# Performance work log

Measured on AMD Instinct MI355X. Metric: run time of the kernel, lower is better.

Reference implementation:

```python
import jax, jax.numpy as jnp
import numpy as np

E = 1024      # embed_dim
H = 16        # num heads
D = E // H    # head_dim = 64
B, T = 4, 2048


def setup_inputs() -> dict:
    key = jax.random.key(0)
    ks = jax.random.split(key, 7)
    hidden_states = jax.random.normal(ks[0], (B, T, E), dtype=jnp.float32)
    # torch Linear weight layout: [out_features, in_features]
    Wqkv = jax.random.normal(ks[1], (3 * E, E), dtype=jnp.float32) * (1.0 / np.sqrt(E))
    bqkv = jax.random.normal(ks[2], (3 * E,), dtype=jnp.float32) * 0.02
    Wproj = jax.random.normal(ks[3], (E, E), dtype=jnp.float32) * (1.0 / np.sqrt(E))
    bproj = jax.random.normal(ks[4], (E,), dtype=jnp.float32) * 0.02
    splat_scale = jax.random.normal(ks[5], (H,), dtype=jnp.float32) * 0.5
    splat_bias = jax.random.normal(ks[6], (H, 1, 1), dtype=jnp.float32) * 0.5
    return {
        'hidden_states': hidden_states,
        'Wqkv': Wqkv, 'bqkv': bqkv,
        'Wproj': Wproj, 'bproj': bproj,
        'splat_scale': splat_scale, 'splat_bias': splat_bias,
    }


def reference(hidden_states, Wqkv, bqkv, Wproj, bproj, splat_scale, splat_bias):
    b, t, _ = hidden_states.shape
    scale_factor = 1.0 / np.sqrt(D)

    qkv = hidden_states @ Wqkv.T + bqkv                    # [B,T,3E]
    q, k, v = jnp.split(qkv, 3, axis=-1)
    # [B,H,T,D]
    q = q.reshape(b, t, H, D).transpose(0, 2, 1, 3)
    k = k.reshape(b, t, H, D).transpose(0, 2, 1, 3)
    v = v.reshape(b, t, H, D).transpose(0, 2, 1, 3)

    scores = jnp.einsum('bhqd,bhkd->bhqk', q * scale_factor, k)  # [B,H,T,T]

    s = (1.0 + 0.01 * jnp.tanh(splat_scale)).reshape(1, H, 1, 1)
    bsp = (0.001 * jnp.tanh(splat_bias)).reshape(1, H, 1, 1)
    scores = s * scores + bsp

    causal = jnp.tril(jnp.ones((t, t), dtype=bool))
    scores = jnp.where(causal, scores, jnp.float32(-1e9))

    attn = jax.nn.softmax(scores, axis=-1)                 # dropout = identity (eval)
    out = jnp.einsum('bhqk,bhkd->bhqd', attn, v)
    out = out.transpose(0, 2, 1, 3).reshape(b, t, E)
    out = out @ Wproj.T + bproj
    return out
```

## Files before the change

kernel.cpp:

```cpp
#include <hip/hip_runtime.h>
#include <stdint.h>

#define BB 4
#define TT 2048
#define EE 1024
#define HH 16
#define DD 64
#define MM (BB*TT)
#define NQKV (3*EE)

typedef __bf16 bf16_t;
typedef bf16_t bf16x8 __attribute__((ext_vector_type(8)));
typedef short  s16x4  __attribute__((ext_vector_type(4)));
typedef float  floatx4 __attribute__((ext_vector_type(4)));

__device__ __forceinline__ unsigned short f2bf(float f) {
    unsigned int u = __float_as_uint(f);
    u = (u + 0x7FFFu + ((u >> 16) & 1u)) >> 16;
    return (unsigned short)u;
}

__device__ __forceinline__ void load_lds16(const void* g, void* l) {
    __builtin_amdgcn_global_load_lds(
        (const __attribute__((address_space(1))) unsigned int*)g,
        (__attribute__((address_space(3))) unsigned int*)l, 16, 0, 0);
}

__global__ void cvt_f32_bf16(const float* __restrict__ in,
                             unsigned short* __restrict__ out, int n) {
    int i = (blockIdx.x * 256 + threadIdx.x) * 4;
    if (i + 3 < n) {
        float4 v = *reinterpret_cast<const float4*>(in + i);
        ushort4 o;
        o.x = f2bf(v.x); o.y = f2bf(v.y); o.z = f2bf(v.z); o.w = f2bf(v.w);
        *reinterpret_cast<ushort4*>(out + i) = o;
    }
}

#define VW(N) asm volatile("s_waitcnt vmcnt(" #N ")" ::: "memory")
#define BARX() do { __builtin_amdgcn_s_barrier(); asm volatile("" ::: "memory"); } while (0)
#define FR(p, t) (*reinterpret_cast<const bf16x8*>((p) + (t) * 512))
#define MFMA1(mi, ni, av, bv) \
    acc[mi][ni] = __builtin_amdgcn_mfma_f32_16x16x32_bf16(av, bv, acc[mi][ni], 0, 0, 0)
#define MFMA_BLK(M0) do { \
    MFMA1(M0+0,0,a0,b0); MFMA1(M0+0,1,a0,b1); MFMA1(M0+0,2,a0,b2); MFMA1(M0+0,3,a0,b3); \
    MFMA1(M0+1,0,a1,b0); MFMA1(M0+1,1,a1,b1); MFMA1(M0+1,2,a1,b2); MFMA1(M0+1,3,a1,b3); \
    MFMA1(M0+2,0,a2,b0); MFMA1(M0+2,1,a2,b1); MFMA1(M0+2,2,a2,b2); MFMA1(M0+2,3,a2,b3); \
    MFMA1(M0+3,0,a3,b0); MFMA1(M0+3,1,a3,b1); MFMA1(M0+3,2,a3,b2); MFMA1(M0+3,3,a3,b3); \
} while (0)
#define STEP_A(kt_, h_) do { \
    const unsigned short* _g = Ag + (kt_) * 64 + (h_) * 32; \
    unsigned short* _l = (unsigned short*)&As[(2*(kt_)+(h_)) & 3][w * 512]; \
    load_lds16(_g, _l); \
    load_lds16(_g + (size_t)128 * 1024, _l + 4096); \
} while (0)
#define STEP_B(kt_, h_) do { \
    const unsigned short* _g = Bg + (kt_) * 64 + (h_) * 32; \
    unsigned short* _l = (unsigned short*)&Bs[(2*(kt_)+(h_)) & 3][w * 512]; \
    load_lds16(_g, _l); \
    load_lds16(_g + (size_t)128 * 1024, _l + 4096); \
} while (0)
#define TILE_BODY(kt_, W1CODE, W3CODE, DOISS) do { \
    const int _s0 = (2 * (kt_)) & 3; \
    const unsigned short* _ap0 = &As[_s0][aoff]; \
    const unsigned short* _bp0 = &Bs[_s0][boff]; \
    const unsigned short* _ap1 = &As[_s0 + 1][aoff]; \
    const unsigned short* _bp1 = &Bs[_s0 + 1][boff]; \
    bf16x8 a0, a1, a2, a3, b0, b1, b2, b3; \
    a0 = FR(_ap0, 0); a1 = FR(_ap0, 1); a2 = FR(_ap0, 2); a3 = FR(_ap0, 3); \
    b0 = FR(_bp0, 0); b1 = FR(_bp0, 1); b2 = FR(_bp0, 2); b3 = FR(_bp0, 3); \
    BARX(); __builtin_amdgcn_s_setprio(1); MFMA_BLK(0); __builtin_amdgcn_s_setprio(0); BARX(); \
    a0 = FR(_ap0, 4); a1 = FR(_ap0, 5); a2 = FR(_ap0, 6); a3 = FR(_ap0, 7); \
    BARX(); __builtin_amdgcn_s_setprio(1); MFMA_BLK(4); __builtin_amdgcn_s_setprio(0); W1CODE; BARX(); \
    a0 = FR(_ap1, 0); a1 = FR(_ap1, 1); a2 = FR(_ap1, 2); a3 = FR(_ap1, 3); \
    b0 = FR(_bp1, 0); b1 = FR(_bp1, 1); b2 = FR(_bp1, 2); b3 = FR(_bp1, 3); \
    BARX(); __builtin_amdgcn_s_setprio(1); \
    if (DOISS) { STEP_A((kt_) + 2, 0); STEP_B((kt_) + 2, 0); } \
    MFMA_BLK(0); __builtin_amdgcn_s_setprio(0); BARX(); \
    a0 = FR(_ap1, 4); a1 = FR(_ap1, 5); a2 = FR(_ap1, 6); a3 = FR(_ap1, 7); \
    BARX(); __builtin_amdgcn_s_setprio(1); \
    if (DOISS) { STEP_A((kt_) + 2, 1); STEP_B((kt_) + 2, 1); } \
    MFMA_BLK(4); __builtin_amdgcn_s_setprio(0); W3CODE; BARX(); \
} while (0)

template<int N, int EPI>
__global__ __launch_bounds__(512, 2) void gemm256(
    const unsigned short* __restrict__ A,
    const unsigned short* __restrict__ Bw,
    const float* __restrict__ bias,
    const float* __restrict__ sscale,
    unsigned short* __restrict__ Qb,
    unsigned short* __restrict__ Kb,
    unsigned short* __restrict__ Vtb,
    float* __restrict__ Cout)
{
    __shared__ __align__(16) unsigned short As[4][8192];
    __shared__ __align__(16) unsigned short Bs[4][8192];

    const int tid  = threadIdx.x;
    const int lane = tid & 63;
    const int w    = tid >> 6;
    const int quad = lane >> 4;
    const int l16  = lane & 15;

    const int nwg = (int)gridDim.x;
    const int wg  = ((int)blockIdx.x & 7) * (nwg >> 3) + ((int)blockIdx.x >> 3);
    const int nbx = N / 256;
    const int m0  = (wg / nbx) * 256;
    const int n0  = (wg % nbx) * 256;

    const int wm = (w >> 2) * 128;
    const int wn = (w & 3) * 64;

    const unsigned short* Ag = A  + (size_t)(m0 + 16 * w + l16) * 1024 + quad * 8;
    const unsigned short* Bg = Bw + (size_t)(n0 + 16 * w + l16) * 1024 + quad * 8;

    const int aoff = (wm >> 4) * 512 + lane * 8;
    const int boff = (wn >> 4) * 512 + lane * 8;

    floatx4 acc[8][4] = {};

    STEP_A(0, 0); STEP_B(0, 0); STEP_A(0, 1); STEP_B(0, 1);
    STEP_A(1, 0); STEP_B(1, 0); STEP_A(1, 1); STEP_B(1, 1);
    VW(12); BARX();

#pragma unroll 2
    for (int kt = 0; kt < 14; ++kt) {
        TILE_BODY(kt, VW(8), VW(12), 1);
    }
    TILE_BODY(14, VW(8), VW(4), 0);
    TILE_BODY(15, VW(0), (void)0, 0);

    if (EPI == 0) {
        const int colb  = n0 + wn;
        const int which = colb >> 10;
#pragma unroll
        for (int nt = 0; nt < 4; ++nt) {
            const int col = colb + nt * 16 + l16;
            const int e = col & 1023;
            const int hh = e >> 6, d = e & 63;
            const float bsv = bias[col];
            float qs = 0.f;
            if (which == 0) qs = (1.0f + 0.01f * tanhf(sscale[hh])) * 0.125f;
#pragma unroll
            for (int mt = 0; mt < 8; ++mt) {
                const int rowb = m0 + wm + mt * 16 + quad * 4;
#pragma unroll
                for (int r = 0; r < 4; ++r) {
                    const int m = rowb + r;
                    const int b = m >> 11, t = m & 2047;
                    const size_t bh = (size_t)(b * HH + hh);
                    float v = acc[mt][nt][r] + bsv;
                    if (which == 0) {
                        Qb[(bh * TT + t) * DD + d] = f2bf(v * qs);
                    } else if (which == 1) {
                        Kb[(bh * TT + t) * DD + d] = f2bf(v);
                    } else {
                        Vtb[(bh * DD + d) * TT + t] = f2bf(v);
                    }
                }
            }
        }
    } else {
#pragma unroll
        for (int mt = 0; mt < 8; ++mt) {
            const int rowb = m0 + wm + mt * 16 + quad * 4;
#pragma unroll
            for (int nt = 0; nt < 4; ++nt) {
                const int col = n0 + wn + nt * 16 + l16;
                const float bsv = bias[col];
#pragma unroll
                for (int r = 0; r < 4; ++r)
                    Cout[(size_t)(rowb + r) * N + col] = acc[mt][nt][r] + bsv;
            }
        }
    }
}

#define LP 72
__global__ __launch_bounds__(256, 4) void flash_attn(
    const unsigned short* __restrict__ Qb,
    const unsigned short* __restrict__ Kb,
    const unsigned short* __restrict__ Vtb,
    unsigned short* __restrict__ Ob)
{
    __shared__ __align__(16) unsigned short Ks[2][64 * LP];
    __shared__ __align__(16) unsigned short Vs[2][64 * LP];

    const int tid  = threadIdx.x;
    const int lane = tid & 63;
    const int w    = tid >> 6;
    const int quad = lane >> 4;
    const int l16  = lane & 15;
    const int i    = blockIdx.x;
    const int bh   = i & 63;
    const int qt   = 31 - (i >> 6);
    const int row0 = qt * 64 + w * 16;

    const unsigned short* qbase = &Qb[((size_t)bh * TT + row0 + l16) * DD + quad * 8];
    const bf16x8 qf0 = *reinterpret_cast<const bf16x8*>(qbase);
    const bf16x8 qf1 = *reinterpret_cast<const bf16x8*>(qbase + 32);

    const s16x4 vones = { (short)0x3F80, (short)0x3F80, (short)0x3F80, (short)0x3F80 };

    floatx4 o[4] = {};
    floatx4 o1 = {};

    const int srow = tid >> 3;
    const int scol = (tid & 7) * 8;
    const size_t kgbase = ((size_t)bh * TT + srow) * DD + scol;
    const size_t vgbase = ((size_t)bh * DD + srow) * TT + scol;

    uint4 kr0 = *reinterpret_cast<const uint4*>(&Kb[kgbase]);
    uint4 kr1 = *reinterpret_cast<const uint4*>(&Kb[kgbase + 32 * DD]);
    uint4 vr0 = *reinterpret_cast<const uint4*>(&Vtb[vgbase]);
    uint4 vr1 = *reinterpret_cast<const uint4*>(&Vtb[vgbase + 32 * TT]);

    for (int kt = 0; kt <= qt; ++kt) {
        const int buf = kt & 1;
        *reinterpret_cast<uint4*>(&Ks[buf][srow * LP + scol]) = kr0;
        *reinterpret_cast<uint4*>(&Ks[buf][(srow + 32) * LP + scol]) = kr1;
        *reinterpret_cast<uint4*>(&Vs[buf][srow * LP + scol]) = vr0;
        *reinterpret_cast<uint4*>(&Vs[buf][(srow + 32) * LP + scol]) = vr1;
        __syncthreads();

        if (kt < qt) {
            size_t ko = kgbase + (size_t)(kt + 1) * 64 * DD;
            size_t vo = vgbase + (size_t)(kt + 1) * 64;
            kr0 = *reinterpret_cast<const uint4*>(&Kb[ko]);
            kr1 = *reinterpret_cast<const uint4*>(&Kb[ko + 32 * DD]);
            vr0 = *reinterpret_cast<const uint4*>(&Vtb[vo]);
            vr1 = *reinterpret_cast<const uint4*>(&Vtb[vo + 32 * TT]);
        }

        const int keyb = kt * 64 + quad * 4;
        const int qr0  = row0 + l16;
        const bool diag = (kt == qt);

#pragma unroll
        for (int ntk = 0; ntk < 4; ++ntk) {
            const unsigned short* krow = &Ks[buf][(ntk * 16 + l16) * LP + quad * 8];
            bf16x8 kf0 = *reinterpret_cast<const bf16x8*>(krow);
            bf16x8 kf1 = *reinterpret_cast<const bf16x8*>(krow + 32);

            floatx4 st = {0.f, 0.f, 0.f, 0.f};
            st = __builtin_amdgcn_mfma_f32_16x16x32_bf16(kf0, qf0, st, 0, 0, 0);
            st = __builtin_amdgcn_mfma_f32_16x16x32_bf16(kf1, qf1, st, 0, 0, 0);

            s16x4 pf;
#pragma unroll
            for (int r = 0; r < 4; ++r) {
                float p = __expf(st[r]);
                pf[r] = (short)((!diag || (keyb + ntk * 16 + r <= qr0)) ? f2bf(p) : 0);
            }

            o1 = __builtin_amdgcn_mfma_f32_16x16x16bf16_1k(pf, vones, o1, 0, 0, 0);
#pragma unroll
            for (int dt = 0; dt < 4; ++dt) {
                s16x4 vf = *reinterpret_cast<const s16x4*>(
                    &Vs[buf][(dt * 16 + l16) * LP + ntk * 16 + quad * 4]);
                o[dt] = __builtin_amdgcn_mfma_f32_16x16x16bf16_1k(pf, vf, o[dt], 0, 0, 0);
            }
        }
    }

    const int b = bh >> 4, h = bh & 15;
#pragma unroll
    for (int r = 0; r < 4; ++r) {
        int q = row0 + quad * 4 + r;
        float rl = __builtin_amdgcn_rcpf(o1[r]);
#pragma unroll
        for (int dt = 0; dt < 4; ++dt)
            Ob[((size_t)(b * TT + q)) * EE + h * DD + dt * 16 + l16] =
                f2bf(o[dt][r] * rl);
    }
}

extern "C" void kernel_launch(void* const* d_in, const int* in_sizes, int n_in,
                              void* d_out, int out_size, void* d_ws, size_t ws_size,
                              hipStream_t stream) {
    const float* hs    = (const float*)d_in[0];
    const float* Wqkv  = (const float*)d_in[1];
    const float* bqkv  = (const float*)d_in[2];
    const float* Wproj = (const float*)d_in[3];
    const float* bproj = (const float*)d_in[4];
    const float* ss    = (const float*)d_in[5];
    float* out = (float*)d_out;

    char* p = (char*)d_ws;
    unsigned short* hsb    = (unsigned short*)p; p += (size_t)MM * EE * 2;
    unsigned short* wqkvb  = (unsigned short*)p; p += (size_t)NQKV * EE * 2;
    unsigned short* wprojb = (unsigned short*)p; p += (size_t)EE * EE * 2;
    unsigned short* Qb     = (unsigned short*)p; p += (size_t)BB*HH*TT*DD * 2;
    unsigned short* Kb     = (unsigned short*)p; p += (size_t)BB*HH*TT*DD * 2;
    unsigned short* Vtb    = (unsigned short*)p; p += (size_t)BB*HH*TT*DD * 2;

    cvt_f32_bf16<<<(MM * EE) / 1024, 256, 0, stream>>>(hs, hsb, MM * EE);
    cvt_f32_bf16<<<(NQKV * EE) / 1024, 256, 0, stream>>>(Wqkv, wqkvb, NQKV * EE);
    cvt_f32_bf16<<<(EE * EE) / 1024, 256, 0, stream>>>(Wproj, wprojb, EE * EE);

    gemm256<NQKV, 0><<<dim3((MM / 256) * (NQKV / 256)), 512, 0, stream>>>(
        hsb, wqkvb, bqkv, ss, Qb, Kb, Vtb, nullptr);

    flash_attn<<<dim3(2048), 256, 0, stream>>>(Qb, Kb, Vtb, hsb);

    gemm256<EE, 1><<<dim3((MM / 256) * (EE / 256)), 512, 0, stream>>>(
        hsb, wprojb, bproj, nullptr, nullptr, nullptr, nullptr, out);
}
```

Baseline: 330.8 us.

## Shrink GEMM tile to 256x128 with triple-buffered LDS and register fragment prefetch

The GEMM tile shrinks from 256x256 to 256x128, so the grid doubles and each wave computes a 64x64 sub-tile. The LDS pipeline moves from double to triple buffering, and A/B fragments are double-buffered in registers so the next half-step's LDS reads overlap the current MFMAs. Each half-step now needs one barrier instead of four. The smaller tile raises global and LDS traffic per FLOP, but is meant to improve wave occupancy and latency hiding.

```diff
diff --git a/kernel.cpp b/kernel.cpp
--- a/kernel.cpp
+++ b/kernel.cpp
@@ -39,48 +39,40 @@
 
 #define VW(N) asm volatile("s_waitcnt vmcnt(" #N ")" ::: "memory")
 #define BARX() do { __builtin_amdgcn_s_barrier(); asm volatile("" ::: "memory"); } while (0)
-#define FR(p, t) (*reinterpret_cast<const bf16x8*>((p) + (t) * 512))
+#define FRv(p, t) (*reinterpret_cast<const bf16x8*>((p) + (t) * 512))
+#define SLOT(kt) (((kt) % 3) * 2)
 #define MFMA1(mi, ni, av, bv) \
     acc[mi][ni] = __builtin_amdgcn_mfma_f32_16x16x32_bf16(av, bv, acc[mi][ni], 0, 0, 0)
-#define MFMA_BLK(M0) do { \
-    MFMA1(M0+0,0,a0,b0); MFMA1(M0+0,1,a0,b1); MFMA1(M0+0,2,a0,b2); MFMA1(M0+0,3,a0,b3); \
-    MFMA1(M0+1,0,a1,b0); MFMA1(M0+1,1,a1,b1); MFMA1(M0+1,2,a1,b2); MFMA1(M0+1,3,a1,b3); \
-    MFMA1(M0+2,0,a2,b0); MFMA1(M0+2,1,a2,b1); MFMA1(M0+2,2,a2,b2); MFMA1(M0+2,3,a2,b3); \
-    MFMA1(M0+3,0,a3,b0); MFMA1(M0+3,1,a3,b1); MFMA1(M0+3,2,a3,b2); MFMA1(M0+3,3,a3,b3); \
+#define MFMA_SET(s) do { \
+    MFMA1(0,0,afr[s][0],bfr[s][0]); MFMA1(0,1,afr[s][0],bfr[s][1]); MFMA1(0,2,afr[s][0],bfr[s][2]); MFMA1(0,3,afr[s][0],bfr[s][3]); \
+    MFMA1(1,0,afr[s][1],bfr[s][0]); MFMA1(1,1,afr[s][1],bfr[s][1]); MFMA1(1,2,afr[s][1],bfr[s][2]); MFMA1(1,3,afr[s][1],bfr[s][3]); \
+    MFMA1(2,0,afr[s][2],bfr[s][0]); MFMA1(2,1,afr[s][2],bfr[s][1]); MFMA1(2,2,afr[s][2],bfr[s][2]); MFMA1(2,3,afr[s][2],bfr[s][3]); \
+    MFMA1(3,0,afr[s][3],bfr[s][0]); MFMA1(3,1,afr[s][3],bfr[s][1]); MFMA1(3,2,afr[s][3],bfr[s][2]); MFMA1(3,3,afr[s][3],bfr[s][3]); \
 } while (0)
-#define STEP_A(kt_, h_) do { \
-    const unsigned short* _g = Ag + (kt_) * 64 + (h_) * 32; \
-    unsigned short* _l = (unsigned short*)&As[(2*(kt_)+(h_)) & 3][w * 512]; \
-    load_lds16(_g, _l); \
-    load_lds16(_g + (size_t)128 * 1024, _l + 4096); \
+#define STAGE_H(kt_, h_) do { \
+    const unsigned short* _ga = Ag + (kt_) * 64 + (h_) * 32; \
+    unsigned short* _la = (unsigned short*)&As[SLOT(kt_) + (h_)][w * 512]; \
+    load_lds16(_ga, _la); \
+    load_lds16(_ga + (size_t)128 * 1024, _la + 4096); \
+    load_lds16(Bg + (kt_) * 64 + (h_) * 32, &Bs[SLOT(kt_) + (h_)][w * 512]); \
 } while (0)
-#define STEP_B(kt_, h_) do { \
-    const unsigned short* _g = Bg + (kt_) * 64 + (h_) * 32; \
-    unsigned short* _l = (unsigned short*)&Bs[(2*(kt_)+(h_)) & 3][w * 512]; \
-    load_lds16(_g, _l); \
-    load_lds16(_g + (size_t)128 * 1024, _l + 4096); \
+#define RDFRAG(st, kt_, h_) do { \
+    const unsigned short* _pa = &As[SLOT(kt_) + (h_)][aoff]; \
+    afr[st][0] = FRv(_pa, 0); afr[st][1] = FRv(_pa, 1); \
+    afr[st][2] = FRv(_pa, 2); afr[st][3] = FRv(_pa, 3); \
+    const unsigned short* _pb = &Bs[SLOT(kt_) + (h_)][boff]; \
+    bfr[st][0] = FRv(_pb, 0); bfr[st][1] = FRv(_pb, 1); \
+    bfr[st][2] = FRv(_pb, 2); bfr[st][3] = FRv(_pb, 3); \
 } while (0)
-#define TILE_BODY(kt_, W1CODE, W3CODE, DOISS) do { \
-    const int _s0 = (2 * (kt_)) & 3; \
-    const unsigned short* _ap0 = &As[_s0][aoff]; \
-    const unsigned short* _bp0 = &Bs[_s0][boff]; \
-    const unsigned short* _ap1 = &As[_s0 + 1][aoff]; \
-    const unsigned short* _bp1 = &Bs[_s0 + 1][boff]; \
-    bf16x8 a0, a1, a2, a3, b0, b1, b2, b3; \
-    a0 = FR(_ap0, 0); a1 = FR(_ap0, 1); a2 = FR(_ap0, 2); a3 = FR(_ap0, 3); \
-    b0 = FR(_bp0, 0); b1 = FR(_bp0, 1); b2 = FR(_bp0, 2); b3 = FR(_bp0, 3); \
-    BARX(); __builtin_amdgcn_s_setprio(1); MFMA_BLK(0); __builtin_amdgcn_s_setprio(0); BARX(); \
-    a0 = FR(_ap0, 4); a1 = FR(_ap0, 5); a2 = FR(_ap0, 6); a3 = FR(_ap0, 7); \
-    BARX(); __builtin_amdgcn_s_setprio(1); MFMA_BLK(4); __builtin_amdgcn_s_setprio(0); W1CODE; BARX(); \
-    a0 = FR(_ap1, 0); a1 = FR(_ap1, 1); a2 = FR(_ap1, 2); a3 = FR(_ap1, 3); \
-    b0 = FR(_bp1, 0); b1 = FR(_bp1, 1); b2 = FR(_bp1, 2); b3 = FR(_bp1, 3); \
-    BARX(); __builtin_amdgcn_s_setprio(1); \
-    if (DOISS) { STEP_A((kt_) + 2, 0); STEP_B((kt_) + 2, 0); } \
-    MFMA_BLK(0); __builtin_amdgcn_s_setprio(0); BARX(); \
-    a0 = FR(_ap1, 4); a1 = FR(_ap1, 5); a2 = FR(_ap1, 6); a3 = FR(_ap1, 7); \
-    BARX(); __builtin_amdgcn_s_setprio(1); \
-    if (DOISS) { STEP_A((kt_) + 2, 1); STEP_B((kt_) + 2, 1); } \
-    MFMA_BLK(4); __builtin_amdgcn_s_setprio(0); W3CODE; BARX(); \
+#define TILE(kt_, VA, VB, DS1, DS0, DRD) do { \
+    VW(VA); BARX();                        \
+    if (DS1) STAGE_H((kt_) + 2, 1); \
+    RDFRAG(1, kt_, 1);                     \
+    __builtin_amdgcn_s_setprio(1); MFMA_SET(0); __builtin_amdgcn_s_setprio(0); \
+    VW(VB); BARX();                        \
+    if (DS0) STAGE_H((kt_) + 3, 0); \
+    if (DRD) RDFRAG(0, (kt_) + 1, 0);      \
+    __builtin_amdgcn_s_setprio(1); MFMA_SET(1); __builtin_amdgcn_s_setprio(0); \
 } while (0)
 
 template<int N, int EPI>
@@ -94,8 +86,8 @@
     unsigned short* __restrict__ Vtb,
     float* __restrict__ Cout)
 {
-    __shared__ __align__(16) unsigned short As[4][8192];
-    __shared__ __align__(16) unsigned short Bs[4][8192];
+    __shared__ __align__(16) unsigned short As[6][8192];
+    __shared__ __align__(16) unsigned short Bs[6][4096];
 
     const int tid  = threadIdx.x;
     const int lane = tid & 63;
@@ -105,31 +97,34 @@
 
     const int nwg = (int)gridDim.x;
     const int wg  = ((int)blockIdx.x & 7) * (nwg >> 3) + ((int)blockIdx.x >> 3);
-    const int nbx = N / 256;
+    const int nbx = N / 128;
     const int m0  = (wg / nbx) * 256;
-    const int n0  = (wg % nbx) * 256;
-
-    const int wm = (w >> 2) * 128;
-    const int wn = (w & 3) * 64;
+    const int n0  = (wg % nbx) * 128;
+
+    const int wm = (w >> 1) * 64;
+    const int wn = (w & 1) * 64;
 
     const unsigned short* Ag = A  + (size_t)(m0 + 16 * w + l16) * 1024 + quad * 8;
     const unsigned short* Bg = Bw + (size_t)(n0 + 16 * w + l16) * 1024 + quad * 8;
 
-    const int aoff = (wm >> 4) * 512 + lane * 8;
-    const int boff = (wn >> 4) * 512 + lane * 8;
-
-    floatx4 acc[8][4] = {};
-
-    STEP_A(0, 0); STEP_B(0, 0); STEP_A(0, 1); STEP_B(0, 1);
-    STEP_A(1, 0); STEP_B(1, 0); STEP_A(1, 1); STEP_B(1, 1);
-    VW(12); BARX();
-
-#pragma unroll 2
-    for (int kt = 0; kt < 14; ++kt) {
-        TILE_BODY(kt, VW(8), VW(12), 1);
-    }
-    TILE_BODY(14, VW(8), VW(4), 0);
-    TILE_BODY(15, VW(0), (void)0, 0);
+    const int aoff = (w >> 1) * 2048 + lane * 8;
+    const int boff = (w & 1) * 2048 + lane * 8;
+
+    bf16x8 afr[2][4], bfr[2][4];
+    floatx4 acc[4][4] = {};
+
+    STAGE_H(0, 0); STAGE_H(0, 1); STAGE_H(1, 0); STAGE_H(1, 1); STAGE_H(2, 0);
+    VW(9); BARX();
+    RDFRAG(0, 0, 0);
+
+#pragma unroll
+    for (int kt = 0; kt < 13; ++kt)
+        TILE(kt, 9, 9, 1, 1, 1);
+    TILE(13, 9, 9, 1, 0, 1);
+    TILE(14, 6, 3, 0, 0, 1);
+    VW(0); BARX();
+    RDFRAG(1, 15, 1);
+    __builtin_amdgcn_s_setprio(1); MFMA_SET(0); MFMA_SET(1); __builtin_amdgcn_s_setprio(0);
 
     if (EPI == 0) {
         const int colb  = n0 + wn;
@@ -143,7 +138,7 @@
             float qs = 0.f;
             if (which == 0) qs = (1.0f + 0.01f * tanhf(sscale[hh])) * 0.125f;
 #pragma unroll
-            for (int mt = 0; mt < 8; ++mt) {
+            for (int mt = 0; mt < 4; ++mt) {
                 const int rowb = m0 + wm + mt * 16 + quad * 4;
 #pragma unroll
                 for (int r = 0; r < 4; ++r) {
@@ -163,7 +158,7 @@
         }
     } else {
 #pragma unroll
-        for (int mt = 0; mt < 8; ++mt) {
+        for (int mt = 0; mt < 4; ++mt) {
             const int rowb = m0 + wm + mt * 16 + quad * 4;
 #pragma unroll
             for (int nt = 0; nt < 4; ++nt) {
@@ -299,11 +294,11 @@
     cvt_f32_bf16<<<(NQKV * EE) / 1024, 256, 0, stream>>>(Wqkv, wqkvb, NQKV * EE);
     cvt_f32_bf16<<<(EE * EE) / 1024, 256, 0, stream>>>(Wproj, wprojb, EE * EE);
 
-    gemm256<NQKV, 0><<<dim3((MM / 256) * (NQKV / 256)), 512, 0, stream>>>(
+    gemm256<NQKV, 0><<<dim3((MM / 256) * (NQKV / 128)), 512, 0, stream>>>(
         hsb, wqkvb, bqkv, ss, Qb, Kb, Vtb, nullptr);
 
     flash_attn<<<dim3(2048), 256, 0, stream>>>(Qb, Kb, Vtb, hsb);
 
-    gemm256<EE, 1><<<dim3((MM / 256) * (EE / 256)), 512, 0, stream>>>(
+    gemm256<EE, 1><<<dim3((MM / 256) * (EE / 128)), 512, 0, stream>>>(
         hsb, wprojb, bproj, nullptr, nullptr, nullptr, nullptr, out);
 }
```

After: 308.0 us. -6.9%, faster.
